# Kernel optimization log

Hardware: AMD Instinct MI355X
Metric: run time of the kernel (lower is better)

## Reference

```python
import jax, jax.numpy as jnp
import numpy as np

ALPHA = 1.0


def setup_inputs() -> dict:
    key = jax.random.key(0)
    ks = jax.random.split(key, 7)
    B, S, IN, OUT = 8, 8192, 1024, 1024
    RANK, DDIM, UDIM = 4, 100, 50
    return {
        "hidden_states": jax.random.normal(ks[0], (B, S, IN), dtype=jnp.float32),
        "W": jax.random.normal(ks[1], (OUT, IN), dtype=jnp.float32) * 0.02,
        "b": jax.random.normal(ks[2], (OUT,), dtype=jnp.float32) * 0.02,
        "lora_down": jax.random.normal(ks[3], (RANK, DDIM), dtype=jnp.float32) * 0.1,
        "lora_up": jax.random.normal(ks[4], (UDIM, RANK), dtype=jnp.float32) * 0.1,
        "down_aux": jax.random.normal(ks[5], (DDIM, IN), dtype=jnp.float32) * 0.03,
        "up_aux": jax.random.normal(ks[6], (OUT, UDIM), dtype=jnp.float32) * 0.03,
    }


def reference(hidden_states, W, b, lora_down, lora_up, down_aux, up_aux):
    # lilora_weight = up_aux @ lora_up @ lora_down @ down_aux  -> [out, in]
    lilora_weight = up_aux @ (lora_up @ (lora_down @ down_aux))
    base = jnp.einsum("bsi,oi->bso", hidden_states, W) + b
    delta = jnp.einsum("bsi,oi->bso", hidden_states, lilora_weight)
    return base + ALPHA * delta
```

## Files before the change

kernel.cpp:

```cpp
#include <hip/hip_runtime.h>
#include <hip/hip_bf16.h>
#include <stdint.h>

#define ALPHA 1.0f

typedef __attribute__((ext_vector_type(8))) short bf16x8;
typedef __attribute__((ext_vector_type(4))) float f32x4;
typedef unsigned short ushort_t;

__device__ __forceinline__ unsigned short f32_to_bf16_rne(float f) {
    union { float f; unsigned int u; } v; v.f = f;
    unsigned int u = v.u;
    unsigned int r = u + 0x7FFFu + ((u >> 16) & 1u);
    return (unsigned short)(r >> 16);
}

__device__ __forceinline__ unsigned int cvt_pk_bf16(float lo, float hi) {
    unsigned int r;
    asm("v_cvt_pk_bf16_f32 %0, %1, %2" : "=v"(r) : "v"(lo), "v"(hi));
    return r;
}

__device__ __forceinline__ void async_copy16(const void* g, void* l) {
    __builtin_amdgcn_global_load_lds(
        (const __attribute__((address_space(1))) void*)g,
        (__attribute__((address_space(3))) void*)l, 16, 0, 0);
}

template <bool BF16OUT>
__global__ __launch_bounds__(256)
void weff_fused_kernel(const float* __restrict__ W,
                       const float* __restrict__ lora_down,
                       const float* __restrict__ lora_up,
                       const float* __restrict__ down_aux,
                       const float* __restrict__ up_aux,
                       void* __restrict__ weff) {
    int o = blockIdx.x;
    int i0 = threadIdx.x * 4;

    float fac[4] = {0.f, 0.f, 0.f, 0.f};
    for (int u = 0; u < 50; ++u) {
        float ua = up_aux[o * 50 + u] * ALPHA;
#pragma unroll
        for (int r = 0; r < 4; ++r) fac[r] += ua * lora_up[u * 4 + r];
    }

    float4 t1[4];
#pragma unroll
    for (int r = 0; r < 4; ++r) t1[r] = make_float4(0.f, 0.f, 0.f, 0.f);
    for (int d = 0; d < 100; ++d) {
        float4 da = *(const float4*)(down_aux + d * 1024 + i0);
#pragma unroll
        for (int r = 0; r < 4; ++r) {
            float ld = lora_down[r * 100 + d];
            t1[r].x += ld * da.x; t1[r].y += ld * da.y;
            t1[r].z += ld * da.z; t1[r].w += ld * da.w;
        }
    }

    float4 acc = *(const float4*)(W + (long)o * 1024 + i0);
#pragma unroll
    for (int r = 0; r < 4; ++r) {
        acc.x += fac[r] * t1[r].x; acc.y += fac[r] * t1[r].y;
        acc.z += fac[r] * t1[r].z; acc.w += fac[r] * t1[r].w;
    }

    if (BF16OUT) {
        ushort4 rr;
        rr.x = f32_to_bf16_rne(acc.x); rr.y = f32_to_bf16_rne(acc.y);
        rr.z = f32_to_bf16_rne(acc.z); rr.w = f32_to_bf16_rne(acc.w);
        *(ushort4*)((ushort_t*)weff + (long)o * 1024 + i0) = rr;
    } else {
        *(float4*)((float*)weff + (long)o * 1024 + i0) = acc;
    }
}

#define BMM 256
#define BNN 256
#define BKK 64

__global__ __launch_bounds__(512, 2)
void gemm_fused_kernel(const float* __restrict__ A,
                       const ushort_t* __restrict__ Bt,
                       const float* __restrict__ bias,
                       float* __restrict__ C, int M, int N, int K) {
    __shared__ __align__(16) ushort_t Ab[2][BMM * BKK];
    __shared__ __align__(16) ushort_t Bb[2][BNN * BKK];

    int nTilesN = N / BNN;
    int nwg = gridDim.x;
    int bid = blockIdx.x;
    int swz = bid;
    if ((nwg & 7) == 0) {
        int cpx = nwg >> 3;
        swz = (bid & 7) * cpx + (bid >> 3);
    }
    int tm = swz / nTilesN;
    int tn = swz % nTilesN;
    const long rowA0 = (long)tm * BMM;
    const long colB0 = (long)tn * BNN;

    int tid = threadIdx.x;
    int lane = tid & 63;
    int wave = tid >> 6;
    int wr = wave >> 2;
    int wc = wave & 3;

    int amrow[2], amcol[2], amlds[2];
#pragma unroll
    for (int q = 0; q < 2; ++q) {
        int p = q * 512 + tid;
        amrow[q] = p >> 3;
        amcol[q] = p & 7;
        amlds[q] = amcol[q] ^ (amrow[q] & 7);
    }

    int prow[2], pcg[2];
#pragma unroll
    for (int q = 0; q < 2; ++q) {
        int pc = q * 512 + tid;
        prow[q] = pc >> 3;
        pcg[q] = (pc & 7) ^ (prow[q] & 7);
    }

    int fr = lane & 15;
    int h4 = lane >> 4;
    int s7 = fr & 7;
    int aoff = (wr * 128 + fr) * 64;
    int boff = (wc * 64 + fr) * 64;
    int ck[2] = { (h4 ^ s7) * 8, ((4 + h4) ^ s7) * 8 };

    f32x4 acc[8][4];
#pragma unroll
    for (int m = 0; m < 8; ++m)
#pragma unroll
        for (int n = 0; n < 4; ++n) acc[m][n] = (f32x4)(0.0f);

    const int nIter = K / BKK;

    float4 vA0[2], vA1[2];

    auto loadAhalf = [&](int kt, int h) {
        const float* src = A + (rowA0 + h * 128) * (long)K + kt * BKK;
#pragma unroll
        for (int q = 0; q < 2; ++q) {
            const float* gp = src + (long)amrow[q] * K + amcol[q] * 8;
            vA0[q] = ((const float4*)gp)[0];
            vA1[q] = ((const float4*)gp)[1];
        }
    };
    auto writeAhalf = [&](int h, int bufsel) {
        ushort_t* dst = &Ab[bufsel][h * 8192];
#pragma unroll
        for (int q = 0; q < 2; ++q) {
            uint4 w;
            w.x = cvt_pk_bf16(vA0[q].x, vA0[q].y);
            w.y = cvt_pk_bf16(vA0[q].z, vA0[q].w);
            w.z = cvt_pk_bf16(vA1[q].x, vA1[q].y);
            w.w = cvt_pk_bf16(vA1[q].z, vA1[q].w);
            *(uint4*)(dst + amrow[q] * 64 + amlds[q] * 8) = w;
        }
    };
    auto stageB = [&](int kt, int h, int bufsel) {
        const ushort_t* src = Bt + (colB0 + h * 128) * (long)K + kt * BKK;
        ushort_t* dst = &Bb[bufsel][h * 8192 + wave * 512];
#pragma unroll
        for (int q = 0; q < 2; ++q)
            async_copy16(src + (long)prow[q] * K + pcg[q] * 8, dst + q * 4096);
    };

    stageB(0, 0, 0); stageB(0, 1, 0);
    loadAhalf(0, 0);
    writeAhalf(0, 0);
    loadAhalf(0, 1);
    writeAhalf(1, 0);
    stageB(1, 0, 1); stageB(1, 1, 1);
    asm volatile("s_waitcnt vmcnt(4) lgkmcnt(0)" ::: "memory");
    __builtin_amdgcn_s_barrier();

#pragma unroll 1
    for (int j = 0; j < nIter; ++j) {
        int c = j & 1, o = c ^ 1;
        const ushort_t* Ac = &Ab[c][0];
        const ushort_t* Bc = &Bb[c][0];
        bool stage1 = (j + 1 < nIter);
        bool stage2 = (j + 2 < nIter);

        bf16x8 aL[4][2], aH[4][2], bL[2][2], bH[2][2];
#pragma unroll
        for (int m = 0; m < 4; ++m)
#pragma unroll
            for (int kk = 0; kk < 2; ++kk)
                aL[m][kk] = *(const bf16x8*)&Ac[aoff + m * 1024 + ck[kk]];
#pragma unroll
        for (int n = 0; n < 2; ++n)
#pragma unroll
            for (int kk = 0; kk < 2; ++kk)
                bL[n][kk] = *(const bf16x8*)&Bc[boff + n * 1024 + ck[kk]];
#pragma unroll
        for (int n = 0; n < 2; ++n)
#pragma unroll
            for (int kk = 0; kk < 2; ++kk)
                bH[n][kk] = *(const bf16x8*)&Bc[boff + (n + 2) * 1024 + ck[kk]];

        if (stage1) loadAhalf(j + 1, 0);

        __builtin_amdgcn_s_setprio(1);
#pragma unroll
        for (int m = 0; m < 4; ++m)
#pragma unroll
            for (int n = 0; n < 2; ++n)
#pragma unroll
                for (int kk = 0; kk < 2; ++kk)
                    acc[m][n] = __builtin_amdgcn_mfma_f32_16x16x32_bf16(
                        aL[m][kk], bL[n][kk], acc[m][n], 0, 0, 0);
        __builtin_amdgcn_s_setprio(0);

        if (stage1) {
            writeAhalf(0, o);
            loadAhalf(j + 1, 1);
        }

        __builtin_amdgcn_s_setprio(1);
#pragma unroll
        for (int m = 0; m < 4; ++m)
#pragma unroll
            for (int n = 0; n < 2; ++n)
#pragma unroll
                for (int kk = 0; kk < 2; ++kk)
                    acc[m][n + 2] = __builtin_amdgcn_mfma_f32_16x16x32_bf16(
                        aL[m][kk], bH[n][kk], acc[m][n + 2], 0, 0, 0);
        __builtin_amdgcn_s_setprio(0);

#pragma unroll
        for (int m = 0; m < 4; ++m)
#pragma unroll
            for (int kk = 0; kk < 2; ++kk)
                aH[m][kk] = *(const bf16x8*)&Ac[aoff + (m + 4) * 1024 + ck[kk]];

        __builtin_amdgcn_s_setprio(1);
#pragma unroll
        for (int m = 0; m < 4; ++m)
#pragma unroll
            for (int n = 0; n < 2; ++n)
#pragma unroll
                for (int kk = 0; kk < 2; ++kk)
                    acc[m + 4][n + 2] = __builtin_amdgcn_mfma_f32_16x16x32_bf16(
                        aH[m][kk], bH[n][kk], acc[m + 4][n + 2], 0, 0, 0);
        __builtin_amdgcn_s_setprio(0);

        if (stage1) writeAhalf(1, o);

        __builtin_amdgcn_s_barrier();

        if (stage2) { stageB(j + 2, 0, c); stageB(j + 2, 1, c); }

        __builtin_amdgcn_s_setprio(1);
#pragma unroll
        for (int m = 0; m < 4; ++m)
#pragma unroll
            for (int n = 0; n < 2; ++n)
#pragma unroll
                for (int kk = 0; kk < 2; ++kk)
                    acc[m + 4][n] = __builtin_amdgcn_mfma_f32_16x16x32_bf16(
                        aH[m][kk], bL[n][kk], acc[m + 4][n], 0, 0, 0);
        __builtin_amdgcn_s_setprio(0);

        if (stage2) {
            asm volatile("s_waitcnt vmcnt(4) lgkmcnt(0)" ::: "memory");
        } else {
            asm volatile("s_waitcnt vmcnt(0) lgkmcnt(0)" ::: "memory");
        }
        __builtin_amdgcn_s_barrier();
    }

    int ccol = lane & 15;
    int crow = (lane >> 4) * 4;
#pragma unroll
    for (int m = 0; m < 8; ++m) {
        long grow = rowA0 + wr * 128 + m * 16 + crow;
#pragma unroll
        for (int n = 0; n < 4; ++n) {
            long gcol = colB0 + wc * 64 + n * 16 + ccol;
            float bb = bias[gcol];
#pragma unroll
            for (int r = 0; r < 4; ++r) {
                C[(grow + r) * N + gcol] = acc[m][n][r] + bb;
            }
        }
    }
}

__global__ __launch_bounds__(256)
void gemm_f32_fallback(const float* __restrict__ A, const float* __restrict__ Bt,
                       const float* __restrict__ bias, float* __restrict__ C,
                       int M, int N, int K) {
    __shared__ float As[64][17];
    __shared__ float Bs[64][17];
    int tilesN = N / 64;
    int tm = blockIdx.x / tilesN;
    int tn = blockIdx.x % tilesN;
    int tid = threadIdx.x;
    int tr = tid / 16, tc = tid % 16;
    float acc[4][4] = {};
    for (int k0 = 0; k0 < K; k0 += 16) {
        for (int t = tid; t < 64 * 16; t += 256) {
            int r = t / 16, c = t % 16;
            As[r][c] = A[((long)tm * 64 + r) * K + k0 + c];
            Bs[r][c] = Bt[((long)tn * 64 + r) * K + k0 + c];
        }
        __syncthreads();
#pragma unroll
        for (int kk = 0; kk < 16; ++kk) {
            float av[4], bv[4];
#pragma unroll
            for (int i = 0; i < 4; ++i) av[i] = As[tr * 4 + i][kk];
#pragma unroll
            for (int j = 0; j < 4; ++j) bv[j] = Bs[tc * 4 + j][kk];
#pragma unroll
            for (int i = 0; i < 4; ++i)
#pragma unroll
                for (int j = 0; j < 4; ++j) acc[i][j] += av[i] * bv[j];
        }
        __syncthreads();
    }
#pragma unroll
    for (int i = 0; i < 4; ++i) {
        long row = (long)tm * 64 + tr * 4 + i;
#pragma unroll
        for (int j = 0; j < 4; ++j) {
            long col = (long)tn * 64 + tc * 4 + j;
            C[row * N + col] = acc[i][j] + bias[col];
        }
    }
}

extern "C" void kernel_launch(void* const* d_in, const int* in_sizes, int n_in,
                              void* d_out, int out_size, void* d_ws, size_t ws_size,
                              hipStream_t stream) {
    const float* hs        = (const float*)d_in[0];
    const float* W         = (const float*)d_in[1];
    const float* b         = (const float*)d_in[2];
    const float* lora_down = (const float*)d_in[3];
    const float* lora_up   = (const float*)d_in[4];
    const float* down_aux  = (const float*)d_in[5];
    const float* up_aux    = (const float*)d_in[6];
    float* out = (float*)d_out;

    const int K = 1024;
    const int N = 1024;
    const int M = in_sizes[0] / K;

    char* ws = (char*)d_ws;
    const size_t NEED_FAST = 2 * 1024 * 1024;

    if (ws_size >= NEED_FAST && (M % BMM) == 0) {
        ushort_t* weff = (ushort_t*)ws;
        weff_fused_kernel<true><<<N, 256, 0, stream>>>(W, lora_down, lora_up,
                                                       down_aux, up_aux, weff);
        int grid = (M / BMM) * (N / BNN);
        gemm_fused_kernel<<<grid, 512, 0, stream>>>(hs, weff, b, out, M, N, K);
    } else {
        float* weff = (float*)ws;
        weff_fused_kernel<false><<<N, 256, 0, stream>>>(W, lora_down, lora_up,
                                                        down_aux, up_aux, weff);
        int grid = (M / 64) * (N / 64);
        gemm_f32_fallback<<<grid, 256, 0, stream>>>(hs, weff, b, out, M, N, K);
    }
}
```

Baseline: 229.3 us.

## Prefetch fp32 A tiles two iterations ahead into dedicated register buffers

The fp32 A-tile global loads now run two k-iterations ahead, issued alongside the async B staging, and are held in two separate register sets, one per half. Before, each A half was loaded only one iteration ahead, inside the MFMA sequence. The aim is to hide global-load latency for the A operand behind a full iteration of MFMA work. The bH LDS reads are also moved later so they overlap with the A writes, and the waitcnt thresholds are raised to match the larger number of loads in flight. The cost is 16 more VGPRs per thread for the extra float4 buffers, which could lower occupancy or cause spills given the already large accumulator array.

```diff
diff --git a/kernel.cpp b/kernel.cpp
--- a/kernel.cpp
+++ b/kernel.cpp
@@ -138,26 +138,47 @@
 
     const int nIter = K / BKK;
 
-    float4 vA0[2], vA1[2];
-
-    auto loadAhalf = [&](int kt, int h) {
-        const float* src = A + (rowA0 + h * 128) * (long)K + kt * BKK;
+    float4 vP0[2], vP1[2], vQ0[2], vQ1[2];
+
+    auto loadAh0 = [&](int kt) {
+        const float* src = A + rowA0 * (long)K + kt * BKK;
 #pragma unroll
         for (int q = 0; q < 2; ++q) {
             const float* gp = src + (long)amrow[q] * K + amcol[q] * 8;
-            vA0[q] = ((const float4*)gp)[0];
-            vA1[q] = ((const float4*)gp)[1];
-        }
-    };
-    auto writeAhalf = [&](int h, int bufsel) {
-        ushort_t* dst = &Ab[bufsel][h * 8192];
+            vP0[q] = ((const float4*)gp)[0];
+            vP1[q] = ((const float4*)gp)[1];
+        }
+    };
+    auto loadAh1 = [&](int kt) {
+        const float* src = A + (rowA0 + 128) * (long)K + kt * BKK;
+#pragma unroll
+        for (int q = 0; q < 2; ++q) {
+            const float* gp = src + (long)amrow[q] * K + amcol[q] * 8;
+            vQ0[q] = ((const float4*)gp)[0];
+            vQ1[q] = ((const float4*)gp)[1];
+        }
+    };
+    auto writeAh0 = [&](int bufsel) {
+        ushort_t* dst = &Ab[bufsel][0];
 #pragma unroll
         for (int q = 0; q < 2; ++q) {
             uint4 w;
-            w.x = cvt_pk_bf16(vA0[q].x, vA0[q].y);
-            w.y = cvt_pk_bf16(vA0[q].z, vA0[q].w);
-            w.z = cvt_pk_bf16(vA1[q].x, vA1[q].y);
-            w.w = cvt_pk_bf16(vA1[q].z, vA1[q].w);
+            w.x = cvt_pk_bf16(vP0[q].x, vP0[q].y);
+            w.y = cvt_pk_bf16(vP0[q].z, vP0[q].w);
+            w.z = cvt_pk_bf16(vP1[q].x, vP1[q].y);
+            w.w = cvt_pk_bf16(vP1[q].z, vP1[q].w);
+            *(uint4*)(dst + amrow[q] * 64 + amlds[q] * 8) = w;
+        }
+    };
+    auto writeAh1 = [&](int bufsel) {
+        ushort_t* dst = &Ab[bufsel][8192];
+#pragma unroll
+        for (int q = 0; q < 2; ++q) {
+            uint4 w;
+            w.x = cvt_pk_bf16(vQ0[q].x, vQ0[q].y);
+            w.y = cvt_pk_bf16(vQ0[q].z, vQ0[q].w);
+            w.z = cvt_pk_bf16(vQ1[q].x, vQ1[q].y);
+            w.w = cvt_pk_bf16(vQ1[q].z, vQ1[q].w);
             *(uint4*)(dst + amrow[q] * 64 + amlds[q] * 8) = w;
         }
     };
@@ -169,13 +190,13 @@
             async_copy16(src + (long)prow[q] * K + pcg[q] * 8, dst + q * 4096);
     };
 
+    loadAh0(0); loadAh1(0);
     stageB(0, 0, 0); stageB(0, 1, 0);
-    loadAhalf(0, 0);
-    writeAhalf(0, 0);
-    loadAhalf(0, 1);
-    writeAhalf(1, 0);
+    writeAh0(0);
+    writeAh1(0);
+    loadAh0(1); loadAh1(1);
     stageB(1, 0, 1); stageB(1, 1, 1);
-    asm volatile("s_waitcnt vmcnt(4) lgkmcnt(0)" ::: "memory");
+    asm volatile("s_waitcnt vmcnt(12) lgkmcnt(0)" ::: "memory");
     __builtin_amdgcn_s_barrier();
 
 #pragma unroll 1
@@ -197,13 +218,6 @@
 #pragma unroll
             for (int kk = 0; kk < 2; ++kk)
                 bL[n][kk] = *(const bf16x8*)&Bc[boff + n * 1024 + ck[kk]];
-#pragma unroll
-        for (int n = 0; n < 2; ++n)
-#pragma unroll
-            for (int kk = 0; kk < 2; ++kk)
-                bH[n][kk] = *(const bf16x8*)&Bc[boff + (n + 2) * 1024 + ck[kk]];
-
-        if (stage1) loadAhalf(j + 1, 0);
 
         __builtin_amdgcn_s_setprio(1);
 #pragma unroll
@@ -216,10 +230,13 @@
                         aL[m][kk], bL[n][kk], acc[m][n], 0, 0, 0);
         __builtin_amdgcn_s_setprio(0);
 
-        if (stage1) {
-            writeAhalf(0, o);
-            loadAhalf(j + 1, 1);
-        }
+        if (stage1) writeAh0(o);
+
+#pragma unroll
+        for (int n = 0; n < 2; ++n)
+#pragma unroll
+            for (int kk = 0; kk < 2; ++kk)
+                bH[n][kk] = *(const bf16x8*)&Bc[boff + (n + 2) * 1024 + ck[kk]];
 
         __builtin_amdgcn_s_setprio(1);
 #pragma unroll
@@ -249,11 +266,14 @@
                         aH[m][kk], bH[n][kk], acc[m + 4][n + 2], 0, 0, 0);
         __builtin_amdgcn_s_setprio(0);
 
-        if (stage1) writeAhalf(1, o);
+        if (stage1) writeAh1(o);
 
         __builtin_amdgcn_s_barrier();
 
-        if (stage2) { stageB(j + 2, 0, c); stageB(j + 2, 1, c); }
+        if (stage2) {
+            loadAh0(j + 2); loadAh1(j + 2);
+            stageB(j + 2, 0, c); stageB(j + 2, 1, c);
+        }
 
         __builtin_amdgcn_s_setprio(1);
 #pragma unroll
@@ -267,7 +287,7 @@
         __builtin_amdgcn_s_setprio(0);
 
         if (stage2) {
-            asm volatile("s_waitcnt vmcnt(4) lgkmcnt(0)" ::: "memory");
+            asm volatile("s_waitcnt vmcnt(12) lgkmcnt(0)" ::: "memory");
         } else {
             asm volatile("s_waitcnt vmcnt(0) lgkmcnt(0)" ::: "memory");
         }
```

Measured after the change: 247.8 us. +8.1%, slower.
